# Kernel tuning notes

Hardware: AMD Instinct MI355X
Metric: run time of the kernel (lower is better)

Reference implementation:

```python
import jax, jax.numpy as jnp
import numpy as np

# dims: batch, seq, d_model, heads, n_buckets, n_hashes, d_ff
B, S, D, H, NB, R, DFF = 2, 4096, 1024, 16, 64, 4, 4096
DH = D // H          # head dim
C = S // NB          # attention chunk length after bucket sort
NCH = S // C         # number of chunks


def layernorm(x, g, b):
    m = x.mean(-1, keepdims=True)
    v = ((x - m) ** 2).mean(-1, keepdims=True)
    return (x - m) / jnp.sqrt(v + 1e-5) * g + b


def lsh_attention(x, Wqk, Wv, Wo, rot):
    Bx, Sx, _ = x.shape
    # shared QK projection (Reformer-style), separate V
    qk = (x @ Wqk).reshape(Bx, Sx, H, DH).transpose(0, 2, 1, 3)  # [B,H,S,dh]
    v = (x @ Wv).reshape(Bx, Sx, H, DH).transpose(0, 2, 1, 3)
    # random-rotation LSH: rot [dh, R, NB//2]
    rotated = jnp.einsum('bhsd,drk->rbhsk', qk, rot)
    buckets = jnp.argmax(jnp.concatenate([rotated, -rotated], -1), -1)  # [R,B,H,S]
    scale = DH ** -0.5
    pos = jnp.arange(Sx)

    def one_round(b_r):  # b_r: [B,H,S] bucket ids for one hash round
        order = jnp.argsort(b_r * Sx + pos, axis=-1)   # stable sort by bucket
        inv = jnp.argsort(order, axis=-1)
        sqk = jnp.take_along_axis(qk, order[..., None], 2)
        sv = jnp.take_along_axis(v, order[..., None], 2)
        sb = jnp.take_along_axis(b_r, order, -1)
        q_c = sqk.reshape(Bx, H, NCH, C, DH)
        # keys are L2-normalized shared qk
        k_c = (sqk / (jnp.linalg.norm(sqk, axis=-1, keepdims=True) + 1e-6)).reshape(Bx, H, NCH, C, DH)
        v_c = sv.reshape(Bx, H, NCH, C, DH)
        ext = lambda t: jnp.concatenate([t, jnp.roll(t, 1, axis=2)], axis=3)  # look back 1 chunk
        k_e, v_e = ext(k_c), ext(v_c)
        b_c = sb.reshape(Bx, H, NCH, C)
        b_e = jnp.concatenate([b_c, jnp.roll(b_c, 1, axis=2)], 3)
        p_c = order.reshape(Bx, H, NCH, C)
        p_e = jnp.concatenate([p_c, jnp.roll(p_c, 1, axis=2)], 3)
        s = jnp.einsum('bhnqd,bhnkd->bhnqk', q_c, k_e) * scale  # [B,H,nch,C,2C]
        s = jnp.where(b_c[..., :, None] == b_e[..., None, :], s, -1e9)   # only same bucket
        s = jnp.where(p_c[..., :, None] == p_e[..., None, :], -1e5, s)   # discourage self
        l = jax.scipy.special.logsumexp(s, -1)
        o = jnp.einsum('bhnqk,bhnkd->bhnqd', jax.nn.softmax(s, -1), v_e)
        o = o.reshape(Bx, H, Sx, DH)
        l = l.reshape(Bx, H, Sx)
        return jnp.take_along_axis(o, inv[..., None], 2), jnp.take_along_axis(l, inv, -1)

    o_all, l_all = jax.vmap(one_round)(buckets)        # [R,B,H,S,dh], [R,B,H,S]
    w = jax.nn.softmax(l_all, axis=0)[..., None]       # weight rounds by logsumexp
    out = (o_all * w).sum(0).transpose(0, 2, 1, 3).reshape(Bx, Sx, D)
    return out @ Wo


def feedforward(x, W1, b1, W2, b2):
    # chunked FF in the original only tiles the sequence dim; math is identical
    return jax.nn.relu(x @ W1 + b1) @ W2 + b2


def setup_inputs() -> dict:
    key = jax.random.key(0)
    ks = jax.random.split(key, 10)
    n = jax.random.normal
    return {
        'x1': n(ks[0], (B, S, D), jnp.float32),
        'x2': n(ks[1], (B, S, D), jnp.float32),
        'Wqk': n(ks[2], (D, D), jnp.float32) * (D ** -0.5),
        'Wv': n(ks[3], (D, D), jnp.float32) * (D ** -0.5),
        'Wo': n(ks[4], (D, D), jnp.float32) * (D ** -0.5),
        'ln1_g': jnp.ones(D, jnp.float32), 'ln1_b': jnp.zeros(D, jnp.float32),
        'W1': n(ks[5], (D, DFF), jnp.float32) * (D ** -0.5), 'bf1': jnp.zeros(DFF, jnp.float32),
        'W2': n(ks[6], (DFF, D), jnp.float32) * (DFF ** -0.5), 'bf2': jnp.zeros(D, jnp.float32),
        'ln2_g': jnp.ones(D, jnp.float32), 'ln2_b': jnp.zeros(D, jnp.float32),
        'rot': n(ks[7], (DH, R, NB // 2), jnp.float32),
    }


def reference(x1, x2, Wqk, Wv, Wo, ln1_g, ln1_b, W1, bf1, W2, bf2, ln2_g, ln2_b, rot):
    # reversible block: y1 = x1 + Attn(LN(x2)); y2 = x2 + FF(LN(y1))
    y1 = x1 + lsh_attention(layernorm(x2, ln1_g, ln1_b), Wqk, Wv, Wo, rot)
    y2 = x2 + feedforward(layernorm(y1, ln2_g, ln2_b), W1, bf1, W2, bf2)
    return (y1, y2)
```

## Files before the change

kernel.cpp:

```cpp
#include <hip/hip_runtime.h>
#include <hip/hip_bf16.h>
#include <math.h>

constexpr int CB   = 2;
constexpr int CS   = 4096;
constexpr int CD   = 1024;
constexpr int CH   = 16;
constexpr int CDH  = 64;
constexpr int CR   = 4;
constexpr int CC   = 64;
constexpr int CNCH = 64;
constexpr int CDFF = 4096;
constexpr int CBS  = CB * CS;
constexpr int CBHS = CB * CH * CS;

typedef __attribute__((ext_vector_type(8))) short short8;
typedef __attribute__((ext_vector_type(4))) short short4v;
typedef __attribute__((ext_vector_type(4))) float f32x4;

__device__ inline unsigned short f2bf(float f) {
    __bf16 h = (__bf16)f;
    union { __bf16 h; unsigned short u; } c; c.h = h;
    return c.u;
}
__device__ inline unsigned int cvt2(float a, float b) {
    return (unsigned int)f2bf(a) | ((unsigned int)f2bf(b) << 16);
}
__device__ inline float bf2f(unsigned short h) {
    union { float f; unsigned int u; } a; a.u = ((unsigned int)h) << 16; return a.f;
}

#define AS3 __attribute__((address_space(3)))
#define AS1 __attribute__((address_space(1)))
__device__ inline void gload16(const unsigned short* g, unsigned short* l) {
    __builtin_amdgcn_global_load_lds((const AS1 unsigned int*)g,
                                     (AS3 unsigned int*)l, 16, 0, 0);
}

__device__ inline short8 ld_short8_u(const unsigned short* p) {
    short4v a = *(const short4v*)p;
    short4v b = *(const short4v*)(p + 4);
    short8 r;
    r[0] = a[0]; r[1] = a[1]; r[2] = a[2]; r[3] = a[3];
    r[4] = b[0]; r[5] = b[1]; r[6] = b[2]; r[7] = b[3];
    return r;
}

__global__ __launch_bounds__(256) void ln_kernel(const float* __restrict__ x,
        const float* __restrict__ g, const float* __restrict__ bta,
        unsigned short* __restrict__ out16, unsigned short* __restrict__ out16lo) {
    int row = blockIdx.x;
    int t = threadIdx.x;
    const float* xr = x + (size_t)row * CD;
    float4 v = *(const float4*)(xr + t * 4);
    float s  = v.x + v.y + v.z + v.w;
    float ss = v.x * v.x + v.y * v.y + v.z * v.z + v.w * v.w;
    #pragma unroll
    for (int off = 1; off < 64; off <<= 1) {
        s  += __shfl_xor(s, off);
        ss += __shfl_xor(ss, off);
    }
    __shared__ float ws_[4], wss_[4];
    int wid = t >> 6;
    if ((t & 63) == 0) { ws_[wid] = s; wss_[wid] = ss; }
    __syncthreads();
    s  = ws_[0] + ws_[1] + ws_[2] + ws_[3];
    ss = wss_[0] + wss_[1] + wss_[2] + wss_[3];
    float mean = s * (1.0f / CD);
    float var  = ss * (1.0f / CD) - mean * mean;
    float rstd = rsqrtf(var + 1e-5f);
    float4 gv = *(const float4*)(g + t * 4);
    float4 bv = *(const float4*)(bta + t * 4);
    float4 o;
    o.x = (v.x - mean) * rstd * gv.x + bv.x;
    o.y = (v.y - mean) * rstd * gv.y + bv.y;
    o.z = (v.z - mean) * rstd * gv.z + bv.z;
    o.w = (v.w - mean) * rstd * gv.w + bv.w;
    ushort4 h; h.x = f2bf(o.x); h.y = f2bf(o.y); h.z = f2bf(o.z); h.w = f2bf(o.w);
    *(ushort4*)(out16 + (size_t)row * CD + t * 4) = h;
    if (out16lo) {
        ushort4 lo;
        lo.x = f2bf(o.x - bf2f(h.x)); lo.y = f2bf(o.y - bf2f(h.y));
        lo.z = f2bf(o.z - bf2f(h.z)); lo.w = f2bf(o.w - bf2f(h.w));
        *(ushort4*)(out16lo + (size_t)row * CD + t * 4) = lo;
    }
}

__global__ __launch_bounds__(256) void wtrans_kernel(const float* __restrict__ W,
        unsigned short* __restrict__ WT, unsigned short* __restrict__ WTlo,
        int K, int N) {
    __shared__ float tile[64][65];
    int n0 = blockIdx.x * 64, k0 = blockIdx.y * 64;
    int tid = threadIdx.x;
    int r = tid >> 4, c4 = tid & 15;
    #pragma unroll
    for (int it = 0; it < 4; ++it) {
        int row = r + it * 16;
        float4 v = *(const float4*)(W + (size_t)(k0 + row) * N + n0 + c4 * 4);
        tile[row][c4 * 4 + 0] = v.x; tile[row][c4 * 4 + 1] = v.y;
        tile[row][c4 * 4 + 2] = v.z; tile[row][c4 * 4 + 3] = v.w;
    }
    __syncthreads();
    #pragma unroll
    for (int it = 0; it < 4; ++it) {
        int nrow = r + it * 16;
        float f0 = tile[c4 * 4 + 0][nrow], f1 = tile[c4 * 4 + 1][nrow];
        float f2 = tile[c4 * 4 + 2][nrow], f3 = tile[c4 * 4 + 3][nrow];
        ushort4 h;
        h.x = f2bf(f0); h.y = f2bf(f1); h.z = f2bf(f2); h.w = f2bf(f3);
        *(ushort4*)(WT + (size_t)(n0 + nrow) * K + k0 + c4 * 4) = h;
        if (WTlo) {
            ushort4 lo;
            lo.x = f2bf(f0 - bf2f(h.x)); lo.y = f2bf(f1 - bf2f(h.y));
            lo.z = f2bf(f2 - bf2f(h.z)); lo.w = f2bf(f3 - bf2f(h.w));
            *(ushort4*)(WTlo + (size_t)(n0 + nrow) * K + k0 + c4 * 4) = lo;
        }
    }
}

template<int EPI, int BM, int BK>
__global__ __launch_bounds__(256) void gemm_bf16(const unsigned short* __restrict__ A,
        const unsigned short* __restrict__ BT, const float* __restrict__ bias,
        const float* __restrict__ res, void* __restrict__ outp,
        int M, int N, int K) {
    constexpr int NH  = BK / 32;
    constexpr int SA  = BM / 64;
    constexpr int MI2 = BM / 32;
    __shared__ __align__(16) unsigned short As[NH * BM * 32];
    __shared__ __align__(16) unsigned short Bs[NH * 128 * 32];
    int tid = threadIdx.x;
    int w = tid >> 6, l = tid & 63;
    int nwg = gridDim.x * gridDim.y;
    int lid = blockIdx.y * gridDim.x + blockIdx.x;
    if (!(nwg & 7)) lid = (lid & 7) * (nwg >> 3) + (lid >> 3);
    int m0 = (lid / gridDim.x) * BM, n0 = (lid % gridDim.x) * 128;
    int wm = (w >> 1) * (BM / 2), wn = (w & 1) * 64;

    const unsigned short* gA[SA]; const unsigned short* gB[2];
    unsigned short* ldsA[SA]; unsigned short* ldsB[2];
    int gchunk = (l & 3) ^ ((l >> 3) & 3);
    #pragma unroll
    for (int s = 0; s < SA; ++s) {
        int j = w * SA + s;
        int R = j * 16 + (l >> 2);
        gA[s] = A + (size_t)(m0 + R) * K + gchunk * 8;
        ldsA[s] = As + j * 512;
    }
    #pragma unroll
    for (int s = 0; s < 2; ++s) {
        int j = w * 2 + s;
        int R = j * 16 + (l >> 2);
        gB[s] = BT + (size_t)(n0 + R) * K + gchunk * 8;
        ldsB[s] = Bs + j * 512;
    }
    int p = (l >> 4) ^ (((l & 15) >> 1) & 3);
    int aoff = (wm + (l & 15)) * 32 + p * 8;
    int boff = (wn + (l & 15)) * 32 + p * 8;

    f32x4 acc[MI2][4];
    #pragma unroll
    for (int i = 0; i < MI2; i++)
        #pragma unroll
        for (int j = 0; j < 4; j++) acc[i][j] = (f32x4)(0.f);

    for (int k0 = 0; k0 < K; k0 += BK) {
        #pragma unroll
        for (int h = 0; h < NH; ++h) {
            #pragma unroll
            for (int s = 0; s < SA; ++s)
                gload16(gA[s] + k0 + h * 32, ldsA[s] + h * (BM * 32));
            gload16(gB[0] + k0 + h * 32, ldsB[0] + h * (128 * 32));
            gload16(gB[1] + k0 + h * 32, ldsB[1] + h * (128 * 32));
        }
        __syncthreads();
        #pragma unroll
        for (int h = 0; h < NH; ++h) {
            short8 af[MI2], bf[4];
            #pragma unroll
            for (int im = 0; im < MI2; ++im)
                af[im] = *(const short8*)(As + h * (BM * 32) + aoff + im * 512);
            #pragma unroll
            for (int in = 0; in < 4; ++in)
                bf[in] = *(const short8*)(Bs + h * (128 * 32) + boff + in * 512);
            #pragma unroll
            for (int im = 0; im < MI2; ++im)
                #pragma unroll
                for (int in = 0; in < 4; ++in)
                    acc[im][in] = __builtin_amdgcn_mfma_f32_16x16x32_bf16(
                        af[im], bf[in], acc[im][in], 0, 0, 0);
        }
        __syncthreads();
    }

    float bv[4];
    if (EPI == 1 || EPI == 2) {
        #pragma unroll
        for (int in = 0; in < 4; ++in) bv[in] = bias[n0 + wn + in * 16 + (l & 15)];
    }
    #pragma unroll
    for (int im = 0; im < MI2; ++im) {
        #pragma unroll
        for (int in = 0; in < 4; ++in) {
            int n = n0 + wn + in * 16 + (l & 15);
            #pragma unroll
            for (int r = 0; r < 4; ++r) {
                int m = m0 + wm + im * 16 + (l >> 4) * 4 + r;
                float v = acc[im][in][r];
                if (EPI == 1) {
                    v = fmaxf(v + bv[in], 0.f);
                    ((unsigned short*)outp)[(size_t)m * N + n] = f2bf(v);
                } else if (EPI == 5) {
                    ((unsigned short*)outp)[(size_t)m * N + n] = f2bf(v);
                } else {
                    if (EPI == 2) v += bv[in] + res[(size_t)m * N + n];
                    if (EPI == 3) v += res[(size_t)m * N + n];
                    ((float*)outp)[(size_t)m * N + n] = v;
                }
            }
        }
    }
}

template<int BM>
__global__ __launch_bounds__(256) void gemm_bf16split(
        const unsigned short* __restrict__ Ah, const unsigned short* __restrict__ Al,
        const unsigned short* __restrict__ BTh, const unsigned short* __restrict__ BTl,
        float* __restrict__ outp, unsigned short* __restrict__ out16,
        int M, int N, int K) {
    constexpr int SA  = BM / 64;
    constexpr int MI2 = BM / 32;
    __shared__ __align__(16) unsigned short Ash[BM * 32];
    __shared__ __align__(16) unsigned short Asl[BM * 32];
    __shared__ __align__(16) unsigned short Bsh[128 * 32];
    __shared__ __align__(16) unsigned short Bsl[128 * 32];
    int tid = threadIdx.x;
    int w = tid >> 6, l = tid & 63;
    int nwg = gridDim.x * gridDim.y;
    int lid = blockIdx.y * gridDim.x + blockIdx.x;
    if (!(nwg & 7)) lid = (lid & 7) * (nwg >> 3) + (lid >> 3);
    int m0 = (lid / gridDim.x) * BM, n0 = (lid % gridDim.x) * 128;
    int wm = (w >> 1) * (BM / 2), wn = (w & 1) * 64;

    size_t goffA[SA]; size_t goffB[2];
    unsigned short* ldsAh[SA]; unsigned short* ldsAl[SA];
    unsigned short* ldsBh[2]; unsigned short* ldsBl[2];
    int gchunk = (l & 3) ^ ((l >> 3) & 3);
    #pragma unroll
    for (int s = 0; s < SA; ++s) {
        int j = w * SA + s;
        int R = j * 16 + (l >> 2);
        goffA[s] = (size_t)(m0 + R) * K + gchunk * 8;
        ldsAh[s] = Ash + j * 512; ldsAl[s] = Asl + j * 512;
    }
    #pragma unroll
    for (int s = 0; s < 2; ++s) {
        int j = w * 2 + s;
        int R = j * 16 + (l >> 2);
        goffB[s] = (size_t)(n0 + R) * K + gchunk * 8;
        ldsBh[s] = Bsh + j * 512; ldsBl[s] = Bsl + j * 512;
    }
    int p = (l >> 4) ^ (((l & 15) >> 1) & 3);
    int aoff = (wm + (l & 15)) * 32 + p * 8;
    int boff = (wn + (l & 15)) * 32 + p * 8;

    f32x4 acc[MI2][4];
    #pragma unroll
    for (int i = 0; i < MI2; i++)
        #pragma unroll
        for (int j = 0; j < 4; j++) acc[i][j] = (f32x4)(0.f);

    for (int k0 = 0; k0 < K; k0 += 32) {
        #pragma unroll
        for (int s = 0; s < SA; ++s) {
            gload16(Ah + goffA[s] + k0, ldsAh[s]);
            gload16(Al + goffA[s] + k0, ldsAl[s]);
        }
        #pragma unroll
        for (int s = 0; s < 2; ++s) {
            gload16(BTh + goffB[s] + k0, ldsBh[s]);
            gload16(BTl + goffB[s] + k0, ldsBl[s]);
        }
        __syncthreads();
        short8 afh[MI2], afl[MI2], bfh[4], bfl[4];
        #pragma unroll
        for (int im = 0; im < MI2; ++im) {
            afh[im] = *(const short8*)(Ash + aoff + im * 512);
            afl[im] = *(const short8*)(Asl + aoff + im * 512);
        }
        #pragma unroll
        for (int in = 0; in < 4; ++in) {
            bfh[in] = *(const short8*)(Bsh + boff + in * 512);
            bfl[in] = *(const short8*)(Bsl + boff + in * 512);
        }
        #pragma unroll
        for (int im = 0; im < MI2; ++im)
            #pragma unroll
            for (int in = 0; in < 4; ++in) {
                acc[im][in] = __builtin_amdgcn_mfma_f32_16x16x32_bf16(
                    afh[im], bfh[in], acc[im][in], 0, 0, 0);
                acc[im][in] = __builtin_amdgcn_mfma_f32_16x16x32_bf16(
                    afl[im], bfh[in], acc[im][in], 0, 0, 0);
                acc[im][in] = __builtin_amdgcn_mfma_f32_16x16x32_bf16(
                    afh[im], bfl[in], acc[im][in], 0, 0, 0);
            }
        __syncthreads();
    }

    #pragma unroll
    for (int im = 0; im < MI2; ++im)
        #pragma unroll
        for (int in = 0; in < 4; ++in) {
            int n = n0 + wn + in * 16 + (l & 15);
            #pragma unroll
            for (int r = 0; r < 4; ++r) {
                int m = m0 + wm + im * 16 + (l >> 4) * 4 + r;
                float v = acc[im][in][r];
                outp[(size_t)m * N + n] = v;
                out16[(size_t)m * N + n] = f2bf(v);
            }
        }
}

template<int EPI>
__global__ __launch_bounds__(256) void gemm_f32(const float* __restrict__ A,
        const float* __restrict__ W, float* __restrict__ out,
        int M, int N, int K) {
    __shared__ __align__(16) float As[16][132];
    __shared__ __align__(16) float Bs[16][132];
    int tid = threadIdx.x;
    int n0 = blockIdx.x * 128;
    int m0 = blockIdx.y * 128;
    int ty = tid >> 4, tx = tid & 15;
    float acc[8][8];
    #pragma unroll
    for (int i = 0; i < 8; i++)
        #pragma unroll
        for (int j = 0; j < 8; j++) acc[i][j] = 0.f;

    for (int k0 = 0; k0 < K; k0 += 16) {
        #pragma unroll
        for (int it = 0; it < 2; ++it) {
            int f4 = tid + it * 256;
            int row = f4 >> 2, c4 = f4 & 3;
            float4 av = *(const float4*)(A + (size_t)(m0 + row) * K + k0 + c4 * 4);
            As[c4 * 4 + 0][row] = av.x;
            As[c4 * 4 + 1][row] = av.y;
            As[c4 * 4 + 2][row] = av.z;
            As[c4 * 4 + 3][row] = av.w;
        }
        #pragma unroll
        for (int it = 0; it < 2; ++it) {
            int f4 = tid + it * 256;
            int kr = f4 >> 5, c4 = f4 & 31;
            *(float4*)(&Bs[kr][c4 * 4]) =
                *(const float4*)(W + (size_t)(k0 + kr) * N + n0 + c4 * 4);
        }
        __syncthreads();
        #pragma unroll
        for (int kk = 0; kk < 16; ++kk) {
            float4 a0 = *(const float4*)(&As[kk][ty * 8]);
            float4 a1 = *(const float4*)(&As[kk][ty * 8 + 4]);
            float4 b0 = *(const float4*)(&Bs[kk][tx * 8]);
            float4 b1 = *(const float4*)(&Bs[kk][tx * 8 + 4]);
            float am[8] = {a0.x, a0.y, a0.z, a0.w, a1.x, a1.y, a1.z, a1.w};
            float bn[8] = {b0.x, b0.y, b0.z, b0.w, b1.x, b1.y, b1.z, b1.w};
            #pragma unroll
            for (int i = 0; i < 8; i++)
                #pragma unroll
                for (int j = 0; j < 8; j++)
                    acc[i][j] = fmaf(am[i], bn[j], acc[i][j]);
        }
        __syncthreads();
    }

    if (EPI == 4) {
        int* ibuck = (int*)out;
        int q = tx & 3, r = tx >> 2;
        #pragma unroll
        for (int i = 0; i < 8; i++) {
            int m = m0 + ty * 8 + i;
            float bestP = -3.4e38f, bestN = -3.4e38f;
            int biP = 0, biN = 0;
            #pragma unroll
            for (int j = 0; j < 8; j++) {
                float v = acc[i][j];
                if ( v > bestP) { bestP =  v; biP = q * 8 + j; }
                if (-v > bestN) { bestN = -v; biN = q * 8 + j; }
            }
            #pragma unroll
            for (int off = 1; off < 4; off <<= 1) {
                float oP = __shfl_xor(bestP, off); int oiP = __shfl_xor(biP, off);
                float oN = __shfl_xor(bestN, off); int oiN = __shfl_xor(biN, off);
                if (oP > bestP || (oP == bestP && oiP < biP)) { bestP = oP; biP = oiP; }
                if (oN > bestN || (oN == bestN && oiN < biN)) { bestN = oN; biN = oiN; }
            }
            if (q == 0) {
                int bi = (bestP >= bestN) ? biP : (biN + 32);
                int hh = m & 15, ss2 = (m >> 4) & (CS - 1), bb2 = m >> 16;
                ibuck[((size_t)((r * CB + bb2) * CH + hh)) * CS + ss2] = bi;
            }
        }
        return;
    }

    #pragma unroll
    for (int i = 0; i < 8; i++) {
        int m = m0 + ty * 8 + i;
        #pragma unroll
        for (int j4 = 0; j4 < 2; j4++) {
            int n = n0 + tx * 8 + j4 * 4;
            float4 v;
            v.x = acc[i][j4 * 4 + 0]; v.y = acc[i][j4 * 4 + 1];
            v.z = acc[i][j4 * 4 + 2]; v.w = acc[i][j4 * 4 + 3];
            *(float4*)(out + (size_t)m * N + n) = v;
        }
    }
}

__global__ __launch_bounds__(64) void sort_kernel(const int* __restrict__ buckets,
                                                  int* __restrict__ sorted_pos) {
    int g = blockIdx.x;
    const int* bk = buckets + (size_t)g * CS;
    __shared__ int hist[64][65];
    __shared__ int bstart[64];
    int t = threadIdx.x;
    #pragma unroll
    for (int i = 0; i < 64; i++) hist[t][i] = 0;
    __syncthreads();
    int base = t * 64;
    for (int i = 0; i < 64; i++) { int b = bk[base + i]; hist[t][b]++; }
    __syncthreads();
    int run = 0;
    for (int tt = 0; tt < 64; tt++) {
        int c = hist[tt][t];
        hist[tt][t] = run;
        run += c;
    }
    int x = run;
    #pragma unroll
    for (int off = 1; off < 64; off <<= 1) {
        int y = __shfl_up(x, off);
        if (t >= off) x += y;
    }
    bstart[t] = x - run;
    __syncthreads();
    for (int i = 0; i < 64; i++) {
        int b = bk[base + i];
        int rank = bstart[b] + hist[t][b];
        hist[t][b]++;
        sorted_pos[(size_t)g * CS + rank] = base + i;
    }
}

__global__ __launch_bounds__(256) void attn_kernel(const unsigned short* __restrict__ qk16,
        const unsigned short* __restrict__ v16, const int* __restrict__ buckets,
        const int* __restrict__ sorted, unsigned short* __restrict__ o_all,
        float* __restrict__ l_all) {
    int n  = blockIdx.x;
    int r  = blockIdx.y;
    int bh = blockIdx.z;
    int b = bh >> 4, h = bh & 15;
    int rbh = (r * CB + b) * CH + h;
    int tid = threadIdx.x;
    int w = tid >> 6, l = tid & 63;
    int l4 = l & 15, qd = l >> 4;

    __shared__ int pk[128];
    __shared__ int bkk[128];
    __shared__ __align__(16) unsigned short Ks[128 * 72];
    __shared__ __align__(16) unsigned short Ps[64 * 132];
    __shared__ __align__(16) unsigned short VsT[64 * 132];

    int prev = (n + CNCH - 1) & (CNCH - 1);
    if (tid < 128) {
        int i = tid & 63;
        int ch = (tid < 64) ? n : prev;
        int p = sorted[(size_t)rbh * CS + ch * CC + i];
        pk[tid] = p;
        bkk[tid] = buckets[(size_t)rbh * CS + p];
    }
    __syncthreads();

    const unsigned short* qbase = qk16 + (size_t)b * CS * CD + h * 64;
    const unsigned short* vbase = v16  + (size_t)b * CS * CD + h * 64;

    #pragma unroll
    for (int it = 0; it < 8; ++it) {
        int f4 = tid + it * 256;
        int kk = f4 >> 4, d4 = f4 & 15;
        ushort4 hv = *(const ushort4*)(qbase + (size_t)pk[kk] * CD + d4 * 4);
        float x0 = bf2f(hv.x), x1 = bf2f(hv.y), x2 = bf2f(hv.z), x3 = bf2f(hv.w);
        float ss = x0 * x0 + x1 * x1 + x2 * x2 + x3 * x3;
        ss += __shfl_xor(ss, 1); ss += __shfl_xor(ss, 2);
        ss += __shfl_xor(ss, 4); ss += __shfl_xor(ss, 8);
        float rn = __builtin_amdgcn_rcpf(sqrtf(ss) + 1e-6f);
        uint2 kp;
        kp.x = cvt2(x0 * rn, x1 * rn);
        kp.y = cvt2(x2 * rn, x3 * rn);
        *(uint2*)&Ks[kk * 72 + d4 * 4] = kp;
    }
    #pragma unroll
    for (int it = 0; it < 16; ++it) {
        int kkp = w * 16 + it;
        int r0 = pk[2 * kkp], r1 = pk[2 * kkp + 1];
        unsigned int u0 = vbase[(size_t)r0 * CD + l];
        unsigned int u1 = vbase[(size_t)r1 * CD + l];
        *(unsigned int*)&VsT[l * 132 + 2 * kkp] = u0 | (u1 << 16);
    }
    int mstrip = w * 16;
    const unsigned short* qptr = qbase + (size_t)pk[mstrip + l4] * CD + qd * 8;
    short8 afA = *(const short8*)(qptr);
    short8 afB = *(const short8*)(qptr + 32);
    __syncthreads();

    f32x4 sa[8];
    #pragma unroll
    for (int t = 0; t < 8; ++t) sa[t] = (f32x4)(0.f);
    #pragma unroll
    for (int t = 0; t < 8; ++t) {
        const unsigned short* kb = &Ks[(t * 16 + l4) * 72 + qd * 8];
        short8 b0 = *(const short8*)(kb);
        short8 b1 = *(const short8*)(kb + 32);
        sa[t] = __builtin_amdgcn_mfma_f32_16x16x32_bf16(afA, b0, sa[t], 0, 0, 0);
        sa[t] = __builtin_amdgcn_mfma_f32_16x16x32_bf16(afB, b1, sa[t], 0, 0, 0);
    }

    int rowb[4], rowp[4];
    #pragma unroll
    for (int rr = 0; rr < 4; ++rr) {
        int m = mstrip + 4 * qd + rr;
        rowb[rr] = bkk[m]; rowp[rr] = pk[m];
    }
    float mx[4] = {-3.4e38f, -3.4e38f, -3.4e38f, -3.4e38f};
    #pragma unroll
    for (int t = 0; t < 8; ++t) {
        int cb = bkk[t * 16 + l4], cp = pk[t * 16 + l4];
        #pragma unroll
        for (int rr = 0; rr < 4; ++rr) {
            float v = sa[t][rr] * 0.125f;
            if (rowb[rr] != cb) v = -1e9f;
            if (rowp[rr] == cp) v = -1e5f;
            sa[t][rr] = v;
            mx[rr] = fmaxf(mx[rr], v);
        }
    }
    #pragma unroll
    for (int rr = 0; rr < 4; ++rr) {
        mx[rr] = fmaxf(mx[rr], __shfl_xor(mx[rr], 1));
        mx[rr] = fmaxf(mx[rr], __shfl_xor(mx[rr], 2));
        mx[rr] = fmaxf(mx[rr], __shfl_xor(mx[rr], 4));
        mx[rr] = fmaxf(mx[rr], __shfl_xor(mx[rr], 8));
    }
    float sum[4] = {0.f, 0.f, 0.f, 0.f};
    #pragma unroll
    for (int t = 0; t < 8; ++t)
        #pragma unroll
        for (int rr = 0; rr < 4; ++rr) {
            float e = __expf(sa[t][rr] - mx[rr]);
            sa[t][rr] = e;
            sum[rr] += e;
        }
    #pragma unroll
    for (int rr = 0; rr < 4; ++rr) {
        sum[rr] += __shfl_xor(sum[rr], 1);
        sum[rr] += __shfl_xor(sum[rr], 2);
        sum[rr] += __shfl_xor(sum[rr], 4);
        sum[rr] += __shfl_xor(sum[rr], 8);
    }
    if (l4 == 0) {
        #pragma unroll
        for (int rr = 0; rr < 4; ++rr)
            l_all[(size_t)rbh * CS + rowp[rr]] = mx[rr] + __logf(sum[rr]);
    }

    float rs[4];
    #pragma unroll
    for (int rr = 0; rr < 4; ++rr) rs[rr] = __builtin_amdgcn_rcpf(sum[rr]);
    #pragma unroll
    for (int t = 0; t < 8; ++t) {
        unsigned int a01 = cvt2(sa[t][0] * rs[0], sa[t][1] * rs[1]);
        unsigned int a23 = cvt2(sa[t][2] * rs[2], sa[t][3] * rs[3]);
        int base = (mstrip + 4 * qd) * 132 + t * 16 + l4;
        Ps[base]       = (unsigned short)(a01 & 0xffffu);
        Ps[base + 132] = (unsigned short)(a01 >> 16);
        Ps[base + 264] = (unsigned short)(a23 & 0xffffu);
        Ps[base + 396] = (unsigned short)(a23 >> 16);
    }

    f32x4 oa[4];
    #pragma unroll
    for (int nt = 0; nt < 4; ++nt) oa[nt] = (f32x4)(0.f);
    #pragma unroll
    for (int ks = 0; ks < 4; ++ks) {
        short8 ap = ld_short8_u(&Ps[(mstrip + l4) * 132 + ks * 32 + qd * 8]);
        #pragma unroll
        for (int nt = 0; nt < 4; ++nt) {
            short8 bv = ld_short8_u(&VsT[(nt * 16 + l4) * 132 + ks * 32 + qd * 8]);
            oa[nt] = __builtin_amdgcn_mfma_f32_16x16x32_bf16(ap, bv, oa[nt], 0, 0, 0);
        }
    }
    size_t ob = (size_t)rbh * CS;
    #pragma unroll
    for (int nt = 0; nt < 4; ++nt) {
        unsigned int a01 = cvt2(oa[nt][0], oa[nt][1]);
        unsigned int a23 = cvt2(oa[nt][2], oa[nt][3]);
        o_all[(ob + rowp[0]) * CDH + nt * 16 + l4] = (unsigned short)(a01 & 0xffffu);
        o_all[(ob + rowp[1]) * CDH + nt * 16 + l4] = (unsigned short)(a01 >> 16);
        o_all[(ob + rowp[2]) * CDH + nt * 16 + l4] = (unsigned short)(a23 & 0xffffu);
        o_all[(ob + rowp[3]) * CDH + nt * 16 + l4] = (unsigned short)(a23 >> 16);
    }
}

__global__ __launch_bounds__(256) void combine_kernel(const unsigned short* __restrict__ o_all,
        const float* __restrict__ l_all, unsigned short* __restrict__ attnout16) {
    int idx = blockIdx.x * 256 + threadIdx.x;
    int d = idx & 63, bhs = idx >> 6;
    int s2 = bhs & (CS - 1), bh = bhs >> 12, h = bh & 15, b = bh >> 4;
    float lr[4];
    #pragma unroll
    for (int r = 0; r < CR; r++) lr[r] = l_all[(size_t)r * CBHS + bhs];
    float m = fmaxf(fmaxf(lr[0], lr[1]), fmaxf(lr[2], lr[3]));
    float w[4], sum = 0.f;
    #pragma unroll
    for (int r = 0; r < CR; r++) { w[r] = __expf(lr[r] - m); sum += w[r]; }
    float acc = 0.f;
    #pragma unroll
    for (int r = 0; r < CR; r++)
        acc += w[r] * bf2f(o_all[((size_t)r * CBHS + bhs) * CDH + d]);
    acc *= __builtin_amdgcn_rcpf(sum);
    attnout16[((size_t)(b * CS + s2)) * CD + h * 64 + d] = f2bf(acc);
}

extern "C" void kernel_launch(void* const* d_in, const int* in_sizes, int n_in,
                              void* d_out, int out_size, void* d_ws, size_t ws_size,
                              hipStream_t stream) {
    const float* x1   = (const float*)d_in[0];
    const float* x2   = (const float*)d_in[1];
    const float* Wqk  = (const float*)d_in[2];
    const float* Wv   = (const float*)d_in[3];
    const float* Wo   = (const float*)d_in[4];
    const float* ln1g = (const float*)d_in[5];
    const float* ln1b = (const float*)d_in[6];
    const float* W1   = (const float*)d_in[7];
    const float* bf1  = (const float*)d_in[8];
    const float* W2   = (const float*)d_in[9];
    const float* bf2  = (const float*)d_in[10];
    const float* ln2g = (const float*)d_in[11];
    const float* ln2b = (const float*)d_in[12];
    const float* rot  = (const float*)d_in[13];

    unsigned short* bufA16   = (unsigned short*)d_ws;
    unsigned short* bufA16lo = bufA16 + (size_t)CBS * CD;
    float* bufB = (float*)(bufA16lo + (size_t)CBS * CD);
    float* bufC = bufB + (size_t)CBS * CD;
    unsigned short* v16  = (unsigned short*)bufC;
    unsigned short* qk16 = v16 + (size_t)CBS * CD;
    unsigned short* o_all = (unsigned short*)(bufC + (size_t)CBS * CD);
    float* l_all  = (float*)(o_all + (size_t)CR * CBHS * CDH);
    int* buckets  = (int*)(l_all + (size_t)CR * CBHS);
    int* sorted   = buckets + (size_t)CR * CBHS;
    unsigned short* WvT   = (unsigned short*)(sorted + (size_t)CR * CBHS);
    unsigned short* WoT   = WvT + (size_t)CD * CD;
    unsigned short* W1T   = WoT + (size_t)CD * CD;
    unsigned short* W2T   = W1T + (size_t)CD * CDFF;
    unsigned short* WqkTh = W2T + (size_t)CD * CDFF;
    unsigned short* WqkTl = WqkTh + (size_t)CD * CD;
    unsigned short* ffh16 = (unsigned short*)bufB;
    unsigned short* attnout16 = bufA16;
    unsigned short* lnY16 = bufA16;
    float* y1 = (float*)d_out;
    float* y2 = y1 + (size_t)CBS * CD;

    wtrans_kernel<<<dim3(CD / 64, CD / 64), 256, 0, stream>>>(Wqk, WqkTh, WqkTl, CD, CD);
    wtrans_kernel<<<dim3(CD / 64, CD / 64), 256, 0, stream>>>(Wv, WvT, nullptr, CD, CD);
    wtrans_kernel<<<dim3(CD / 64, CD / 64), 256, 0, stream>>>(Wo, WoT, nullptr, CD, CD);
    wtrans_kernel<<<dim3(CDFF / 64, CD / 64), 256, 0, stream>>>(W1, W1T, nullptr, CD, CDFF);
    wtrans_kernel<<<dim3(CD / 64, CDFF / 64), 256, 0, stream>>>(W2, W2T, nullptr, CDFF, CD);
    ln_kernel<<<CBS, 256, 0, stream>>>(x2, ln1g, ln1b, bufA16, bufA16lo);
    gemm_bf16split<64><<<dim3(CD / 128, CBS / 64), 256, 0, stream>>>(
        bufA16, bufA16lo, WqkTh, WqkTl, bufB, qk16, CBS, CD, CD);
    gemm_bf16<5, 64, 64><<<dim3(CD / 128, CBS / 64), 256, 0, stream>>>(
        bufA16, WvT, nullptr, nullptr, v16, CBS, CD, CD);
    gemm_f32<4><<<dim3(1, CBHS / 128), 256, 0, stream>>>(bufB, rot, (float*)buckets, CBHS, 128, 64);
    sort_kernel<<<CR * CB * CH, 64, 0, stream>>>(buckets, sorted);
    attn_kernel<<<dim3(CNCH, CR, CB * CH), 256, 0, stream>>>(qk16, v16, buckets, sorted, o_all, l_all);
    combine_kernel<<<(CBHS * CDH) / 256, 256, 0, stream>>>(o_all, l_all, attnout16);
    gemm_bf16<3, 64, 64><<<dim3(CD / 128, CBS / 64), 256, 0, stream>>>(
        attnout16, WoT, nullptr, x1, y1, CBS, CD, CD);
    ln_kernel<<<CBS, 256, 0, stream>>>(y1, ln2g, ln2b, lnY16, nullptr);
    gemm_bf16<1, 128, 32><<<dim3(CDFF / 128, CBS / 128), 256, 0, stream>>>(
        lnY16, W1T, bf1, nullptr, ffh16, CBS, CDFF, CD);
    gemm_bf16<2, 64, 64><<<dim3(CD / 128, CBS / 64), 256, 0, stream>>>(
        ffh16, W2T, bf2, x2, y2, CBS, CD, CDFF);
}
```

Before: 643.3 us.

## Merge weight transposes, stage sort buckets in LDS, vectorize combine

Folds the five weight-transpose launches into one launch that picks its weight matrix from the block index. The sort kernel now loads bucket ids into padded shared memory with coalesced reads, where before each thread read its own strided slice from global memory twice. The combine kernel has each thread handle four head-dim elements with vector loads and a packed bf16 store, which cuts the thread count and the number of l_all reloads. The main aim is to cut launch overhead and uncoalesced global traffic; the extra shared memory in sort may affect its occupancy.

```diff
diff --git a/kernel.cpp b/kernel.cpp
--- a/kernel.cpp
+++ b/kernel.cpp
@@ -86,11 +86,23 @@
     }
 }
 
-__global__ __launch_bounds__(256) void wtrans_kernel(const float* __restrict__ W,
-        unsigned short* __restrict__ WT, unsigned short* __restrict__ WTlo,
-        int K, int N) {
+__global__ __launch_bounds__(256) void wtrans_all(const float* __restrict__ Wqk,
+        const float* __restrict__ Wv, const float* __restrict__ Wo,
+        const float* __restrict__ W1, const float* __restrict__ W2,
+        unsigned short* __restrict__ WqkTh, unsigned short* __restrict__ WqkTl,
+        unsigned short* __restrict__ WvT, unsigned short* __restrict__ WoT,
+        unsigned short* __restrict__ W1T, unsigned short* __restrict__ W2T) {
+    int bid = blockIdx.x;
+    const float* W; unsigned short* WT; unsigned short* WTlo = nullptr;
+    int K, N, bx, by;
+    if (bid < 256)        { W = Wqk; WT = WqkTh; WTlo = WqkTl; K = CD;   N = CD;   int i = bid;        bx = i & 15; by = i >> 4; }
+    else if (bid < 512)   { W = Wv;  WT = WvT;                 K = CD;   N = CD;   int i = bid - 256;  bx = i & 15; by = i >> 4; }
+    else if (bid < 768)   { W = Wo;  WT = WoT;                 K = CD;   N = CD;   int i = bid - 512;  bx = i & 15; by = i >> 4; }
+    else if (bid < 1792)  { W = W1;  WT = W1T;                 K = CD;   N = CDFF; int i = bid - 768;  bx = i & 63; by = i >> 6; }
+    else                  { W = W2;  WT = W2T;                 K = CDFF; N = CD;   int i = bid - 1792; bx = i & 15; by = i >> 4; }
+
     __shared__ float tile[64][65];
-    int n0 = blockIdx.x * 64, k0 = blockIdx.y * 64;
+    int n0 = bx * 64, k0 = by * 64;
     int tid = threadIdx.x;
     int r = tid >> 4, c4 = tid & 15;
     #pragma unroll
@@ -113,7 +125,7 @@
             ushort4 lo;
             lo.x = f2bf(f0 - bf2f(h.x)); lo.y = f2bf(f1 - bf2f(h.y));
             lo.z = f2bf(f2 - bf2f(h.z)); lo.w = f2bf(f3 - bf2f(h.w));
-            *(ushort4*)(WTlo + (size_t)(n0 + nrow) * K + k0 + c4 * 4) = lo;
+            *(ushort4*)(WqkTl + (size_t)(n0 + nrow) * K + k0 + c4 * 4) = lo;
         }
     }
 }
@@ -423,12 +435,16 @@
     const int* bk = buckets + (size_t)g * CS;
     __shared__ int hist[64][65];
     __shared__ int bstart[64];
+    __shared__ int bkl[64 * 65];
     int t = threadIdx.x;
     #pragma unroll
     for (int i = 0; i < 64; i++) hist[t][i] = 0;
+    for (int i = 0; i < 64; i++) {
+        int p = i * 64 + t;
+        bkl[p + (p >> 6)] = bk[p];
+    }
     __syncthreads();
-    int base = t * 64;
-    for (int i = 0; i < 64; i++) { int b = bk[base + i]; hist[t][b]++; }
+    for (int i = 0; i < 64; i++) { int b = bkl[t * 65 + i]; hist[t][b]++; }
     __syncthreads();
     int run = 0;
     for (int tt = 0; tt < 64; tt++) {
@@ -445,10 +461,10 @@
     bstart[t] = x - run;
     __syncthreads();
     for (int i = 0; i < 64; i++) {
-        int b = bk[base + i];
+        int b = bkl[t * 65 + i];
         int rank = bstart[b] + hist[t][b];
         hist[t][b]++;
-        sorted_pos[(size_t)g * CS + rank] = base + i;
+        sorted_pos[(size_t)g * CS + rank] = t * 64 + i;
     }
 }
 
@@ -614,7 +630,7 @@
 __global__ __launch_bounds__(256) void combine_kernel(const unsigned short* __restrict__ o_all,
         const float* __restrict__ l_all, unsigned short* __restrict__ attnout16) {
     int idx = blockIdx.x * 256 + threadIdx.x;
-    int d = idx & 63, bhs = idx >> 6;
+    int d4 = (idx & 15) * 4, bhs = idx >> 4;
     int s2 = bhs & (CS - 1), bh = bhs >> 12, h = bh & 15, b = bh >> 4;
     float lr[4];
     #pragma unroll
@@ -623,12 +639,18 @@
     float w[4], sum = 0.f;
     #pragma unroll
     for (int r = 0; r < CR; r++) { w[r] = __expf(lr[r] - m); sum += w[r]; }
-    float acc = 0.f;
-    #pragma unroll
-    for (int r = 0; r < CR; r++)
-        acc += w[r] * bf2f(o_all[((size_t)r * CBHS + bhs) * CDH + d]);
-    acc *= __builtin_amdgcn_rcpf(sum);
-    attnout16[((size_t)(b * CS + s2)) * CD + h * 64 + d] = f2bf(acc);
+    float a0 = 0.f, a1 = 0.f, a2 = 0.f, a3 = 0.f;
+    #pragma unroll
+    for (int r = 0; r < CR; r++) {
+        ushort4 ov = *(const ushort4*)&o_all[((size_t)r * CBHS + bhs) * CDH + d4];
+        a0 += w[r] * bf2f(ov.x); a1 += w[r] * bf2f(ov.y);
+        a2 += w[r] * bf2f(ov.z); a3 += w[r] * bf2f(ov.w);
+    }
+    float rsum = __builtin_amdgcn_rcpf(sum);
+    uint2 pk2;
+    pk2.x = cvt2(a0 * rsum, a1 * rsum);
+    pk2.y = cvt2(a2 * rsum, a3 * rsum);
+    *(uint2*)&attnout16[((size_t)(b * CS + s2)) * CD + h * 64 + d4] = pk2;
 }
 
 extern "C" void kernel_launch(void* const* d_in, const int* in_sizes, int n_in,
@@ -671,11 +693,8 @@
     float* y1 = (float*)d_out;
     float* y2 = y1 + (size_t)CBS * CD;
 
-    wtrans_kernel<<<dim3(CD / 64, CD / 64), 256, 0, stream>>>(Wqk, WqkTh, WqkTl, CD, CD);
-    wtrans_kernel<<<dim3(CD / 64, CD / 64), 256, 0, stream>>>(Wv, WvT, nullptr, CD, CD);
-    wtrans_kernel<<<dim3(CD / 64, CD / 64), 256, 0, stream>>>(Wo, WoT, nullptr, CD, CD);
-    wtrans_kernel<<<dim3(CDFF / 64, CD / 64), 256, 0, stream>>>(W1, W1T, nullptr, CD, CDFF);
-    wtrans_kernel<<<dim3(CD / 64, CDFF / 64), 256, 0, stream>>>(W2, W2T, nullptr, CDFF, CD);
+    wtrans_all<<<2816, 256, 0, stream>>>(Wqk, Wv, Wo, W1, W2,
+                                         WqkTh, WqkTl, WvT, WoT, W1T, W2T);
     ln_kernel<<<CBS, 256, 0, stream>>>(x2, ln1g, ln1b, bufA16, bufA16lo);
     gemm_bf16split<64><<<dim3(CD / 128, CBS / 64), 256, 0, stream>>>(
         bufA16, bufA16lo, WqkTh, WqkTl, bufB, qk16, CBS, CD, CD);
@@ -684,7 +703,7 @@
     gemm_f32<4><<<dim3(1, CBHS / 128), 256, 0, stream>>>(bufB, rot, (float*)buckets, CBHS, 128, 64);
     sort_kernel<<<CR * CB * CH, 64, 0, stream>>>(buckets, sorted);
     attn_kernel<<<dim3(CNCH, CR, CB * CH), 256, 0, stream>>>(qk16, v16, buckets, sorted, o_all, l_all);
-    combine_kernel<<<(CBHS * CDH) / 256, 256, 0, stream>>>(o_all, l_all, attnout16);
+    combine_kernel<<<(CBHS * CDH) / 1024, 256, 0, stream>>>(o_all, l_all, attnout16);
     gemm_bf16<3, 64, 64><<<dim3(CD / 128, CBS / 64), 256, 0, stream>>>(
         attnout16, WoT, nullptr, x1, y1, CBS, CD, CD);
     ln_kernel<<<CBS, 256, 0, stream>>>(y1, ln2g, ln2b, lnY16, nullptr);
```

Measured after the change: 643.5 us. Within noise of the previous version (+0.0%).
